# Optimization experiments

Measured on AMD Instinct MI355X. Metric: run time of the kernel, lower is better.

## Reference

```python
import jax, jax.numpy as jnp
import numpy as np

D_MODEL = 256
N_HEADS = 8
D_FF = 1024
N_LAYERS = 6
INPUT_DIM = 2
EPS = 1e-5  # torch LayerNorm default


def _layer_norm(x, g, b):
    m = jnp.mean(x, axis=-1, keepdims=True)
    v = jnp.mean((x - m) ** 2, axis=-1, keepdims=True)
    return (x - m) / jnp.sqrt(v + EPS) * g + b


def setup_inputs() -> dict:
    key = jax.random.key(0)
    ks = jax.random.split(key, 8)
    f32 = jnp.float32

    def w(k, shape, fan_in):
        return jax.random.normal(k, shape, f32) * (1.0 / np.sqrt(fan_in))

    return {
        "x": jax.random.normal(ks[0], (8, 1024, INPUT_DIM), f32),
        "in_w": w(ks[1], (INPUT_DIM, D_MODEL), INPUT_DIM),
        "in_b": jnp.zeros((D_MODEL,), f32),
        "ln1_g": jnp.ones((D_MODEL,), f32),
        "ln1_b": jnp.zeros((D_MODEL,), f32),
        "qkv_w": w(ks[2], (D_MODEL, 3 * D_MODEL), D_MODEL),
        "qkv_b": jnp.zeros((3 * D_MODEL,), f32),
        "out_w": w(ks[3], (D_MODEL, D_MODEL), D_MODEL),
        "out_b": jnp.zeros((D_MODEL,), f32),
        "lna_g": jnp.ones((D_MODEL,), f32),
        "lna_b": jnp.zeros((D_MODEL,), f32),
        "ln2_g": jnp.ones((D_MODEL,), f32),
        "ln2_b": jnp.zeros((D_MODEL,), f32),
        "ff1_w": w(ks[4], (D_MODEL, D_FF), D_MODEL),
        "ff1_b": jnp.zeros((D_FF,), f32),
        "ff2_w": w(ks[5], (D_FF, D_MODEL), D_FF),
        "ff2_b": jnp.zeros((D_MODEL,), f32),
        "lnf_g": jnp.ones((D_MODEL,), f32),
        "lnf_b": jnp.zeros((D_MODEL,), f32),
    }


def reference(x, in_w, in_b, ln1_g, ln1_b, qkv_w, qkv_b, out_w, out_b,
              lna_g, lna_b, ln2_g, ln2_b, ff1_w, ff1_b, ff2_w, ff2_b,
              lnf_g, lnf_b):
    B, L, _ = x.shape
    dk = D_MODEL // N_HEADS
    scale = 1.0 / np.sqrt(dk)
    top_k = max(1, L // 4)

    # sinusoidal positional encoding [L, D]
    pos = jnp.arange(L, dtype=jnp.float32)[:, None]
    div = jnp.exp(jnp.arange(0, D_MODEL, 2, dtype=jnp.float32)
                  * (-np.log(10000.0) / D_MODEL))
    pe = jnp.zeros((L, D_MODEL), jnp.float32)
    pe = pe.at[:, 0::2].set(jnp.sin(pos * div))
    pe = pe.at[:, 1::2].set(jnp.cos(pos * div))

    h = x @ in_w + in_b + pe[None]  # [B, L, D]

    # VoformerEncoder reuses the SAME layer object -> shared weights, 6 passes
    for _ in range(N_LAYERS):
        # --- self-attention sublayer (pre-norm) ---
        s2 = _layer_norm(h, ln1_g, ln1_b)
        qkv = (s2 @ qkv_w + qkv_b).reshape(B, L, 3, N_HEADS, dk)
        q = qkv[:, :, 0].transpose(0, 2, 1, 3)  # [B, H, L, dk]
        k = qkv[:, :, 1].transpose(0, 2, 1, 3)
        v = qkv[:, :, 2].transpose(0, 2, 1, 3)

        scores = jnp.einsum('bhqd,bhkd->bhqk', q, k) * scale  # [B,H,L,L]
        # ProbSparse: keep only the per-row top-k scores
        thr = jax.lax.top_k(scores, top_k)[0][..., -1:]
        sparse = jnp.where(scores >= thr, scores, -jnp.inf)
        attn = jax.nn.softmax(sparse, axis=-1)
        o = jnp.einsum('bhqk,bhkd->bhqd', attn, v)
        o = o.transpose(0, 2, 1, 3).reshape(B, L, D_MODEL)
        o = o @ out_w + out_b
        # InformerAttention applies its own residual + LayerNorm
        attn_out = _layer_norm(o + s2, lna_g, lna_b)
        h = h + attn_out

        # --- FFN sublayer with Volatilite activation ---
        s2 = _layer_norm(h, ln2_g, ln2_b)
        f = s2 @ ff1_w + ff1_b  # [B, L, d_ff]
        mean_f = jnp.mean(f, axis=1, keepdims=True)
        vol = jnp.sqrt(jnp.mean((mean_f - f) ** 2, axis=1, keepdims=True))
        f = f * vol
        f = f @ ff2_w + ff2_b
        h = h + f

    return _layer_norm(h, lnf_g, lnf_b)
```

## Files before the change

kernel.cpp:

```cpp
#include <hip/hip_runtime.h>
#include <hip/hip_bf16.h>
#include <math.h>

#define D_MODEL 256
#define NH 8
#define DFF 1024
#define NLAYERS 6
#define B_ 8
#define L_ 1024
#define NR (B_*L_)
#define TOPK 256
#define LNEPS 1e-5f

typedef __attribute__((ext_vector_type(8))) short bf16x8;
typedef __attribute__((ext_vector_type(4))) float f32x4;

__device__ __forceinline__ float wsum(float v){
  #pragma unroll
  for(int o=32;o>0;o>>=1) v += __shfl_xor(v,o,64);
  return v;
}
__device__ __forceinline__ short f2bf(float x){
  unsigned u = __float_as_uint(x);
  u += 0x7fffu + ((u>>16)&1u);
  return (short)(u>>16);
}
__device__ __forceinline__ float bf2f(short s){
  return __uint_as_float(((unsigned)(unsigned short)s)<<16);
}
__device__ __forceinline__ unsigned pk2bf(float a, float b){
  __hip_bfloat162 h = __float22bfloat162_rn(make_float2(a,b));
  unsigned u; __builtin_memcpy(&u, &h, 4);
  return u;
}
__device__ __forceinline__ float kinvf(int k){
  unsigned u = (k & 0x8000) ? ((unsigned)k ^ 0x8000u) : ((unsigned)k ^ 0xFFFFu);
  return __uint_as_float(u << 16);
}
__device__ __forceinline__ void g2l(const short* g, short* l){
  __builtin_amdgcn_global_load_lds(
      (const __attribute__((address_space(1))) unsigned int*)g,
      (__attribute__((address_space(3))) unsigned int*)l,
      16, 0, 0);
}

__global__ __launch_bounds__(256) void embed_kernel(
    const float* __restrict__ x, const float* __restrict__ in_w,
    const float* __restrict__ in_b, float* __restrict__ h)
{
  int tid = blockIdx.x*256 + threadIdx.x;
  int n  = tid >> 6;
  int d0 = (tid & 63) << 2;
  int l  = n & (L_-1);
  float x0 = x[2*n], x1 = x[2*n+1];
  const float kf = -0.07195578415606394f;
  float pe[4];
  #pragma unroll
  for(int ii=0; ii<2; ++ii){
    int i = (d0>>1) + ii;
    float dv  = expf((float)i * kf);
    float ang = (float)l * dv;
    pe[2*ii]   = sinf(ang);
    pe[2*ii+1] = cosf(ang);
  }
  float4 w0 = *(const float4*)(in_w + d0);
  float4 w1 = *(const float4*)(in_w + D_MODEL + d0);
  float4 bb = *(const float4*)(in_b + d0);
  float4 o;
  o.x = x0*w0.x + x1*w1.x + bb.x + pe[0];
  o.y = x0*w0.y + x1*w1.y + bb.y + pe[1];
  o.z = x0*w0.z + x1*w1.z + bb.z + pe[2];
  o.w = x0*w0.w + x1*w1.w + bb.w + pe[3];
  *(float4*)(h + (size_t)n*D_MODEL + d0) = o;
}

__global__ __launch_bounds__(256) void wcvt(
    const float* __restrict__ W, short* __restrict__ WT, int N, int kshift)
{
  int idx = blockIdx.x*256 + threadIdx.x;
  int K = 1<<kshift;
  if (idx >= N*K) return;
  int n = idx >> kshift, k = idx & (K-1);
  WT[idx] = f2bf(W[(size_t)k*N + n]);
}

template<int OM>
__global__ __launch_bounds__(256) void ln_kernel(
    const float* __restrict__ in, const float* __restrict__ g,
    const float* __restrict__ b, float* __restrict__ out,
    short* __restrict__ outb)
{
  int wave = threadIdx.x >> 6, lane = threadIdx.x & 63;
  int row = blockIdx.x*4 + wave;
  float4 v = ((const float4*)(in + (size_t)row*D_MODEL))[lane];
  float s  = v.x+v.y+v.z+v.w;
  float sq = v.x*v.x+v.y*v.y+v.z*v.z+v.w*v.w;
  s = wsum(s); sq = wsum(sq);
  float mean = s*(1.f/D_MODEL);
  float var  = sq*(1.f/D_MODEL) - mean*mean;
  float rstd = 1.f/sqrtf(var + LNEPS);
  float4 gv = ((const float4*)g)[lane];
  float4 bv = ((const float4*)b)[lane];
  float4 o;
  o.x = (v.x-mean)*rstd*gv.x + bv.x;
  o.y = (v.y-mean)*rstd*gv.y + bv.y;
  o.z = (v.z-mean)*rstd*gv.z + bv.z;
  o.w = (v.w-mean)*rstd*gv.w + bv.w;
  if (OM == 0){
    ((float4*)(out + (size_t)row*D_MODEL))[lane] = o;
  }
  if (OM == 2){
    uint2 pk; pk.x = pk2bf(o.x, o.y); pk.y = pk2bf(o.z, o.w);
    *(uint2*)(outb + (size_t)row*D_MODEL + lane*4) = pk;
  }
}

__global__ __launch_bounds__(256) void lnln_kernel(
    const float* __restrict__ tb,
    const float* __restrict__ ga, const float* __restrict__ ba,
    const float* __restrict__ g2, const float* __restrict__ b2,
    float* __restrict__ h, short* __restrict__ s2b)
{
  int wave = threadIdx.x >> 6, lane = threadIdx.x & 63;
  int row = blockIdx.x*4 + wave;
  float4 v = ((const float4*)(tb + (size_t)row*D_MODEL))[lane];
  float s  = v.x+v.y+v.z+v.w;
  float sq = v.x*v.x+v.y*v.y+v.z*v.z+v.w*v.w;
  s = wsum(s); sq = wsum(sq);
  float mean = s*(1.f/D_MODEL);
  float var  = sq*(1.f/D_MODEL) - mean*mean;
  float rstd = 1.f/sqrtf(var + LNEPS);
  float4 gv = ((const float4*)ga)[lane];
  float4 bv = ((const float4*)ba)[lane];
  float4* hp = (float4*)(h + (size_t)row*D_MODEL) + lane;
  float4 hv = *hp;
  float4 hn;
  hn.x = hv.x + (v.x-mean)*rstd*gv.x + bv.x;
  hn.y = hv.y + (v.y-mean)*rstd*gv.y + bv.y;
  hn.z = hv.z + (v.z-mean)*rstd*gv.z + bv.z;
  hn.w = hv.w + (v.w-mean)*rstd*gv.w + bv.w;
  *hp = hn;
  float s2  = hn.x+hn.y+hn.z+hn.w;
  float sq2 = hn.x*hn.x+hn.y*hn.y+hn.z*hn.z+hn.w*hn.w;
  s2 = wsum(s2); sq2 = wsum(sq2);
  float m2 = s2*(1.f/D_MODEL);
  float v2 = sq2*(1.f/D_MODEL) - m2*m2;
  float r2 = 1.f/sqrtf(v2 + LNEPS);
  float4 g2v = ((const float4*)g2)[lane];
  float4 b2v = ((const float4*)b2)[lane];
  uint2 pk;
  pk.x = pk2bf((hn.x-m2)*r2*g2v.x + b2v.x, (hn.y-m2)*r2*g2v.y + b2v.y);
  pk.y = pk2bf((hn.z-m2)*r2*g2v.z + b2v.z, (hn.w-m2)*r2*g2v.w + b2v.w);
  *(uint2*)(s2b + (size_t)row*D_MODEL + lane*4) = pk;
}

template<int MODE>
__global__ __launch_bounds__(256) void mfma_gemm(
    const short* __restrict__ A, const short* __restrict__ BT,
    const float* __restrict__ bias, const short* __restrict__ residb,
    float* __restrict__ Cf, short* __restrict__ Cb, short* __restrict__ Vt,
    int N, int K)
{
  __shared__ __align__(16) short As[128*32];
  __shared__ __align__(16) short Bs[64*32];
  const int t = threadIdx.x, wv = t>>6, lane = t&63;
  const int r16 = lane&15, quad = lane>>4;
  const int m0 = blockIdx.y*128, n0 = blockIdx.x*64;
  const int ia0 = wv*128 + lane, ia1 = ia0 + 64;
  const int ib  = wv*64 + lane;
  const short* Ab = A  + (size_t)m0*K;
  const short* Bb = BT + (size_t)n0*K;
  const f32x4 z = {0.f,0.f,0.f,0.f};
  f32x4 acc[2][4];
  #pragma unroll
  for (int i=0;i<2;++i)
    #pragma unroll
    for (int j=0;j<4;++j) acc[i][j] = z;

  for (int k0 = 0; k0 < K; k0 += 32){
    __syncthreads();
    g2l(Ab + (size_t)(ia0>>2)*K + k0 + (ia0&3)*8, As + ia0*8);
    g2l(Ab + (size_t)(ia1>>2)*K + k0 + (ia1&3)*8, As + ia1*8);
    g2l(Bb + (size_t)(ib>>2)*K  + k0 + (ib&3)*8,  Bs + ib*8);
    __syncthreads();
    bf16x8 af0 = *(const bf16x8*)(As + ((wv*32      + r16)*32 + quad*8));
    bf16x8 af1 = *(const bf16x8*)(As + ((wv*32 + 16 + r16)*32 + quad*8));
    bf16x8 bf[4];
    #pragma unroll
    for (int ct=0; ct<4; ++ct)
      bf[ct] = *(const bf16x8*)(Bs + ((ct*16 + r16)*32 + quad*8));
    #pragma unroll
    for (int ct=0; ct<4; ++ct){
      acc[0][ct] = __builtin_amdgcn_mfma_f32_16x16x32_bf16(af0, bf[ct], acc[0][ct], 0,0,0);
      acc[1][ct] = __builtin_amdgcn_mfma_f32_16x16x32_bf16(af1, bf[ct], acc[1][ct], 0,0,0);
    }
  }

  #pragma unroll
  for (int rt=0; rt<2; ++rt){
    const int mb = m0 + wv*32 + rt*16 + quad*4;
    #pragma unroll
    for (int ct=0; ct<4; ++ct){
      const int n = n0 + ct*16 + r16;
      const float bv = bias[n];
      if (MODE == 0){
        if (n < 512){
          int region = n>>8, hh = (n>>5)&7, d = n&31;
          #pragma unroll
          for (int r=0;r<4;++r){
            int l = mb + r;
            size_t base = (((size_t)(region*64 + (l>>10)*8 + hh))*1024 + (l&1023))*32 + d;
            Cb[base] = f2bf(acc[rt][ct][r] + bv);
          }
        } else {
          int dv = n - 512, hh = dv>>5, d = dv&31;
          int b = mb>>10, lloc = mb&1023;
          size_t base = (((size_t)(b*8 + hh))*32 + d)*1024 + lloc;
          uint2 pk;
          pk.x = pk2bf(acc[rt][ct][0] + bv, acc[rt][ct][1] + bv);
          pk.y = pk2bf(acc[rt][ct][2] + bv, acc[rt][ct][3] + bv);
          *(uint2*)(Vt + base) = pk;
        }
      } else {
        #pragma unroll
        for (int r=0;r<4;++r){
          size_t off = (size_t)(mb + r)*N + n;
          float c = acc[rt][ct][r] + bv;
          if (MODE == 1) Cf[off] = c + bf2f(residb[off]);
          if (MODE == 2) Cb[off] = f2bf(c);
          if (MODE == 3) Cf[off] += c;
        }
      }
    }
  }
}

__global__ __launch_bounds__(256,5) void attn_mfma(
    const short* __restrict__ qkbf, const short* __restrict__ vT,
    short* __restrict__ ob)
{
  __shared__ __align__(16) short sc16[16*1024];
  const int t = threadIdx.x, wv = t>>6, lane = t&63;
  const int r16 = lane&15, quad = lane>>4;
  const int blk = blockIdx.x;
  const int bh = (blk & 7)*8 + ((blk>>3)&7);
  const int qt = blk >> 6;

  bf16x8 aq = *(const bf16x8*)(qkbf + ((size_t)bh*1024 + qt*16 + r16)*32 + quad*8);
  const short* kb = qkbf + (size_t)(64 + bh)*1024*32;
  short* p0 = sc16 + quad*4096;

  #pragma unroll
  for (int g=0; g<4; ++g){
    bf16x8 bkb[4];
    #pragma unroll
    for (int j=0;j<4;++j)
      bkb[j] = *(const bf16x8*)(kb + (size_t)(wv*256 + (g*4+j)*16 + r16)*32 + quad*8);
    #pragma unroll
    for (int j=0;j<4;++j){
      f32x4 c = {0.f,0.f,0.f,0.f};
      c = __builtin_amdgcn_mfma_f32_16x16x32_bf16(aq, bkb[j], c, 0, 0, 0);
      const int keyq = (wv*256 + (g*4+j)*16 + r16) ^ ((quad&1)<<5);
      unsigned u01 = pk2bf(c[0], c[1]);
      unsigned u23 = pk2bf(c[2], c[3]);
      p0[keyq]               = (short)u01;
      p0[1024 + (keyq ^ 8)]  = (short)(u01>>16);
      p0[2048 + (keyq ^ 16)] = (short)u23;
      p0[3072 + (keyq ^ 24)] = (short)(u23>>16);
    }
  }
  __syncthreads();

  const float SC2 = 0.25500529485087056f;
  float iv0, iv1, iv2, iv3;
  #pragma unroll
  for (int rp=0; rp<2; ++rp){
    const int ra = wv*4 + rp*2;
    const int sa = (ra&7)<<3;
    short* pa = sc16 + ra*1024 + ((2*lane) ^ sa);
    short* pb = sc16 + (ra+1)*1024 + (((2*lane) ^ sa) ^ 8);
    float fa[16], fb[16];
    #pragma unroll
    for (int i=0;i<8;++i){
      unsigned wa = *(const unsigned*)(pa + i*128);
      unsigned wb = *(const unsigned*)(pb + i*128);
      fa[2*i]   = __uint_as_float(wa << 16);
      fa[2*i+1] = __uint_as_float(wa & 0xFFFF0000u);
      fb[2*i]   = __uint_as_float(wb << 16);
      fb[2*i+1] = __uint_as_float(wb & 0xFFFF0000u);
    }
    int loA = 0, loB = 0;
    #pragma unroll
    for (int bit = 15; bit >= 0; --bit){
      const int mA = loA | (1<<bit);
      const int mB = loB | (1<<bit);
      const float tA = kinvf(mA);
      const float tB = kinvf(mB);
      int cA = 0, cB = 0;
      #pragma unroll
      for (int i=0;i<16;++i){
        cA += (int)__popcll(__ballot(fa[i] >= tA));
        cB += (int)__popcll(__ballot(fb[i] >= tB));
      }
      if (cA >= TOPK) loA = mA;
      if (cB >= TOPK) loB = mB;
    }
    const float thrA = kinvf(loA), thrB = kinvf(loB);
    float suma = 0.f, sumb = 0.f;
    unsigned pka[8], pkb[8];
    #pragma unroll
    for (int i=0;i<8;++i){
      float ea0 = (fa[2*i]   >= thrA) ? exp2f(fa[2*i]  *SC2) : 0.f;
      float ea1 = (fa[2*i+1] >= thrA) ? exp2f(fa[2*i+1]*SC2) : 0.f;
      float eb0 = (fb[2*i]   >= thrB) ? exp2f(fb[2*i]  *SC2) : 0.f;
      float eb1 = (fb[2*i+1] >= thrB) ? exp2f(fb[2*i+1]*SC2) : 0.f;
      suma += ea0 + ea1; sumb += eb0 + eb1;
      pka[i] = pk2bf(ea0, ea1);
      pkb[i] = pk2bf(eb0, eb1);
    }
    suma = wsum(suma); sumb = wsum(sumb);
    if (rp == 0){ iv0 = 1.f/suma; iv1 = 1.f/sumb; }
    else        { iv2 = 1.f/suma; iv3 = 1.f/sumb; }
    #pragma unroll
    for (int i=0;i<8;++i){
      *(unsigned*)(pa + i*128) = pka[i];
      *(unsigned*)(pb + i*128) = pkb[i];
    }
  }
  const float invq = (quad==0)?iv0 : (quad==1)?iv1 : (quad==2)?iv2 : iv3;
  __syncthreads();

  const short* vb = vT + (size_t)bh*32*1024;
  const int sA = (r16&7) << 3;
  f32x4 oa0 = {0.f,0.f,0.f,0.f}, oa1 = {0.f,0.f,0.f,0.f};
  #pragma unroll
  for (int g=0; g<4; ++g){
    bf16x8 bvb[4];
    #pragma unroll
    for (int j=0;j<2;++j){
      int k0 = wv*256 + (g*2+j)*32;
      bvb[j*2+0] = *(const bf16x8*)(vb + (size_t)(     r16)*1024 + k0 + quad*8);
      bvb[j*2+1] = *(const bf16x8*)(vb + (size_t)(16 + r16)*1024 + k0 + quad*8);
    }
    #pragma unroll
    for (int j=0;j<2;++j){
      int k0 = wv*256 + (g*2+j)*32;
      bf16x8 af = *(const bf16x8*)(sc16 + r16*1024 + ((k0 + quad*8) ^ sA));
      oa0 = __builtin_amdgcn_mfma_f32_16x16x32_bf16(af, bvb[j*2+0], oa0, 0, 0, 0);
      oa1 = __builtin_amdgcn_mfma_f32_16x16x32_bf16(af, bvb[j*2+1], oa1, 0, 0, 0);
    }
  }
  __syncthreads();
  float* po = (float*)sc16;
  #pragma unroll
  for (int r=0;r<4;++r){
    po[wv*512 + (quad*4+r)*32 +      r16] = oa0[r];
    po[wv*512 + (quad*4+r)*32 + 16 + r16] = oa1[r];
  }
  __syncthreads();
  int e = t*2;
  float v0 = po[e]   + po[512+e]   + po[1024+e]   + po[1536+e];
  float v1 = po[e+1] + po[512+e+1] + po[1024+e+1] + po[1536+e+1];
  int q = e>>5, d = e&31;
  int b = bh>>3, hh = bh&7;
  size_t off = ((size_t)(b*1024 + qt*16 + q))*256 + hh*32 + d;
  *(unsigned*)(ob + off) = pk2bf(v0*invq, v1*invq);
}

__global__ __launch_bounds__(512) void vol_scale(short* __restrict__ f)
{
  __shared__ float ps[8][64], pq[8][64], vs[64];
  int b = blockIdx.x >> 4, cb = blockIdx.x & 15;
  int cl = threadIdx.x & 63, sl = threadIdx.x >> 6;
  int col = cb*64 + cl;
  short* fb = f + (size_t)b*L_*DFF + col;
  float s = 0.f, sq = 0.f;
  for (int l = sl*128; l < sl*128+128; ++l){
    float v = bf2f(fb[(size_t)l*DFF]);
    s += v; sq += v*v;
  }
  ps[sl][cl] = s; pq[sl][cl] = sq;
  __syncthreads();
  if (threadIdx.x < 64){
    float st=0.f, qt=0.f;
    #pragma unroll
    for (int i=0;i<8;++i){ st += ps[i][cl]; qt += pq[i][cl]; }
    float mean = st*(1.f/L_);
    float var  = qt*(1.f/L_) - mean*mean;
    vs[cl] = sqrtf(fmaxf(var, 0.f));
  }
  __syncthreads();
  float vv = vs[cl];
  for (int l = sl*128; l < sl*128+128; ++l){
    size_t o = (size_t)l*DFF;
    fb[o] = f2bf(bf2f(fb[o]) * vv);
  }
}

extern "C" void kernel_launch(void* const* d_in, const int* in_sizes, int n_in,
                              void* d_out, int out_size, void* d_ws, size_t ws_size,
                              hipStream_t stream) {
  const float* x     = (const float*)d_in[0];
  const float* in_w  = (const float*)d_in[1];
  const float* in_b  = (const float*)d_in[2];
  const float* ln1_g = (const float*)d_in[3];
  const float* ln1_b = (const float*)d_in[4];
  const float* qkv_w = (const float*)d_in[5];
  const float* qkv_b = (const float*)d_in[6];
  const float* out_w = (const float*)d_in[7];
  const float* out_b = (const float*)d_in[8];
  const float* lna_g = (const float*)d_in[9];
  const float* lna_b = (const float*)d_in[10];
  const float* ln2_g = (const float*)d_in[11];
  const float* ln2_b = (const float*)d_in[12];
  const float* ff1_w = (const float*)d_in[13];
  const float* ff1_b = (const float*)d_in[14];
  const float* ff2_w = (const float*)d_in[15];
  const float* ff2_b = (const float*)d_in[16];
  const float* lnf_g = (const float*)d_in[17];
  const float* lnf_b = (const float*)d_in[18];
  float* out = (float*)d_out;

  char* ws = (char*)d_ws;
  float* h     = (float*)(ws);
  short* s2b   = (short*)(ws + (size_t)( 8<<20));
  short* qkbf  = (short*)(ws + (size_t)(12<<20));
  short* vTb   = (short*)(ws + (size_t)(20<<20));
  short* ob_b  = (short*)(ws + (size_t)(24<<20));
  short* f     = (short*)(ws + (size_t)(12<<20));
  float* tb    = (float*)(ws + (size_t)(28<<20));
  short* qkvwT = (short*)(ws + (size_t)(36<<20));
  short* outwT = (short*)(ws + (size_t)(36<<20) + 393216);
  short* ff1wT = (short*)(ws + (size_t)(36<<20) + 393216 + 131072);
  short* ff2wT = (short*)(ws + (size_t)(36<<20) + 393216 + 131072 + 524288);

  embed_kernel<<<NR*64/256, 256, 0, stream>>>(x, in_w, in_b, h);
  wcvt<<< 768, 256, 0, stream>>>(qkv_w, qkvwT,  768, 8);
  wcvt<<< 256, 256, 0, stream>>>(out_w, outwT,  256, 8);
  wcvt<<<1024, 256, 0, stream>>>(ff1_w, ff1wT, 1024, 8);
  wcvt<<<1024, 256, 0, stream>>>(ff2_w, ff2wT,  256, 10);

  for (int layer = 0; layer < NLAYERS; ++layer){
    ln_kernel<2><<<NR/4, 256, 0, stream>>>(h, ln1_g, ln1_b, nullptr, s2b);
    {
      dim3 g(768/64, NR/128);
      mfma_gemm<0><<<g, 256, 0, stream>>>(s2b, qkvwT, qkv_b, nullptr,
                                          nullptr, qkbf, vTb, 768, 256);
    }
    attn_mfma<<<64*64, 256, 0, stream>>>(qkbf, vTb, ob_b);
    {
      dim3 g(256/64, NR/128);
      mfma_gemm<1><<<g, 256, 0, stream>>>(ob_b, outwT, out_b, s2b,
                                          tb, nullptr, nullptr, 256, 256);
    }
    lnln_kernel<<<NR/4, 256, 0, stream>>>(tb, lna_g, lna_b, ln2_g, ln2_b, h, s2b);
    {
      dim3 g(1024/64, NR/128);
      mfma_gemm<2><<<g, 256, 0, stream>>>(s2b, ff1wT, ff1_b, nullptr,
                                          nullptr, f, nullptr, 1024, 256);
    }
    vol_scale<<<B_*16, 512, 0, stream>>>(f);
    {
      dim3 g(256/64, NR/128);
      mfma_gemm<3><<<g, 256, 0, stream>>>(f, ff2wT, ff2_b, nullptr,
                                          h, nullptr, nullptr, 256, 1024);
    }
  }
  ln_kernel<0><<<NR/4, 256, 0, stream>>>(h, lnf_g, lnf_b, out, nullptr);
}
```

Before: 1.273 ms.

## Use 8 waves per attention block, one row pair per wave

The attention kernel now launches 512 threads (8 waves) per 16-query tile instead of 256. Each wave handles 128 keys in the score and PV stages and one pair of rows in the top-k/softmax stage, where before it handled two pairs. Normalization is now applied to the probabilities before the PV MFMA rather than to the output. A separate 16KB LDS buffer for the partial-output reduction removes one barrier, at the cost of more shared memory per block and an 8-way reduction done by half the threads.

```diff
diff --git a/kernel.cpp b/kernel.cpp
--- a/kernel.cpp
+++ b/kernel.cpp
@@ -235,11 +235,12 @@
   }
 }
 
-__global__ __launch_bounds__(256,5) void attn_mfma(
+__global__ __launch_bounds__(512,6) void attn_mfma(
     const short* __restrict__ qkbf, const short* __restrict__ vT,
     short* __restrict__ ob)
 {
   __shared__ __align__(16) short sc16[16*1024];
+  __shared__ __align__(16) float po[8*512];
   const int t = threadIdx.x, wv = t>>6, lane = t&63;
   const int r16 = lane&15, quad = lane>>4;
   const int blk = blockIdx.x;
@@ -251,16 +252,16 @@
   short* p0 = sc16 + quad*4096;
 
   #pragma unroll
-  for (int g=0; g<4; ++g){
+  for (int g=0; g<2; ++g){
     bf16x8 bkb[4];
     #pragma unroll
     for (int j=0;j<4;++j)
-      bkb[j] = *(const bf16x8*)(kb + (size_t)(wv*256 + (g*4+j)*16 + r16)*32 + quad*8);
+      bkb[j] = *(const bf16x8*)(kb + (size_t)(wv*128 + (g*4+j)*16 + r16)*32 + quad*8);
     #pragma unroll
     for (int j=0;j<4;++j){
       f32x4 c = {0.f,0.f,0.f,0.f};
       c = __builtin_amdgcn_mfma_f32_16x16x32_bf16(aq, bkb[j], c, 0, 0, 0);
-      const int keyq = (wv*256 + (g*4+j)*16 + r16) ^ ((quad&1)<<5);
+      const int keyq = (wv*128 + (g*4+j)*16 + r16) ^ ((quad&1)<<5);
       unsigned u01 = pk2bf(c[0], c[1]);
       unsigned u23 = pk2bf(c[2], c[3]);
       p0[keyq]               = (short)u01;
@@ -272,10 +273,8 @@
   __syncthreads();
 
   const float SC2 = 0.25500529485087056f;
-  float iv0, iv1, iv2, iv3;
-  #pragma unroll
-  for (int rp=0; rp<2; ++rp){
-    const int ra = wv*4 + rp*2;
+  {
+    const int ra = wv*2;
     const int sa = (ra&7)<<3;
     short* pa = sc16 + ra*1024 + ((2*lane) ^ sa);
     short* pb = sc16 + (ra+1)*1024 + (((2*lane) ^ sa) ^ 8);
@@ -306,65 +305,52 @@
       if (cB >= TOPK) loB = mB;
     }
     const float thrA = kinvf(loA), thrB = kinvf(loB);
+    float ea[16], eb[16];
     float suma = 0.f, sumb = 0.f;
-    unsigned pka[8], pkb[8];
+    #pragma unroll
+    for (int i=0;i<16;++i){
+      ea[i] = (fa[i] >= thrA) ? exp2f(fa[i]*SC2) : 0.f;
+      eb[i] = (fb[i] >= thrB) ? exp2f(fb[i]*SC2) : 0.f;
+      suma += ea[i]; sumb += eb[i];
+    }
+    suma = wsum(suma); sumb = wsum(sumb);
+    const float inva = 1.f/suma, invb = 1.f/sumb;
     #pragma unroll
     for (int i=0;i<8;++i){
-      float ea0 = (fa[2*i]   >= thrA) ? exp2f(fa[2*i]  *SC2) : 0.f;
-      float ea1 = (fa[2*i+1] >= thrA) ? exp2f(fa[2*i+1]*SC2) : 0.f;
-      float eb0 = (fb[2*i]   >= thrB) ? exp2f(fb[2*i]  *SC2) : 0.f;
-      float eb1 = (fb[2*i+1] >= thrB) ? exp2f(fb[2*i+1]*SC2) : 0.f;
-      suma += ea0 + ea1; sumb += eb0 + eb1;
-      pka[i] = pk2bf(ea0, ea1);
-      pkb[i] = pk2bf(eb0, eb1);
-    }
-    suma = wsum(suma); sumb = wsum(sumb);
-    if (rp == 0){ iv0 = 1.f/suma; iv1 = 1.f/sumb; }
-    else        { iv2 = 1.f/suma; iv3 = 1.f/sumb; }
-    #pragma unroll
-    for (int i=0;i<8;++i){
-      *(unsigned*)(pa + i*128) = pka[i];
-      *(unsigned*)(pb + i*128) = pkb[i];
-    }
-  }
-  const float invq = (quad==0)?iv0 : (quad==1)?iv1 : (quad==2)?iv2 : iv3;
+      *(unsigned*)(pa + i*128) = pk2bf(ea[2*i]*inva, ea[2*i+1]*inva);
+      *(unsigned*)(pb + i*128) = pk2bf(eb[2*i]*invb, eb[2*i+1]*invb);
+    }
+  }
   __syncthreads();
 
   const short* vb = vT + (size_t)bh*32*1024;
   const int sA = (r16&7) << 3;
   f32x4 oa0 = {0.f,0.f,0.f,0.f}, oa1 = {0.f,0.f,0.f,0.f};
   #pragma unroll
-  for (int g=0; g<4; ++g){
-    bf16x8 bvb[4];
-    #pragma unroll
-    for (int j=0;j<2;++j){
-      int k0 = wv*256 + (g*2+j)*32;
-      bvb[j*2+0] = *(const bf16x8*)(vb + (size_t)(     r16)*1024 + k0 + quad*8);
-      bvb[j*2+1] = *(const bf16x8*)(vb + (size_t)(16 + r16)*1024 + k0 + quad*8);
-    }
-    #pragma unroll
-    for (int j=0;j<2;++j){
-      int k0 = wv*256 + (g*2+j)*32;
-      bf16x8 af = *(const bf16x8*)(sc16 + r16*1024 + ((k0 + quad*8) ^ sA));
-      oa0 = __builtin_amdgcn_mfma_f32_16x16x32_bf16(af, bvb[j*2+0], oa0, 0, 0, 0);
-      oa1 = __builtin_amdgcn_mfma_f32_16x16x32_bf16(af, bvb[j*2+1], oa1, 0, 0, 0);
-    }
-  }
-  __syncthreads();
-  float* po = (float*)sc16;
+  for (int j=0;j<4;++j){
+    int k0 = wv*128 + j*32;
+    bf16x8 b0 = *(const bf16x8*)(vb + (size_t)(     r16)*1024 + k0 + quad*8);
+    bf16x8 b1 = *(const bf16x8*)(vb + (size_t)(16 + r16)*1024 + k0 + quad*8);
+    bf16x8 af = *(const bf16x8*)(sc16 + r16*1024 + ((k0 + quad*8) ^ sA));
+    oa0 = __builtin_amdgcn_mfma_f32_16x16x32_bf16(af, b0, oa0, 0, 0, 0);
+    oa1 = __builtin_amdgcn_mfma_f32_16x16x32_bf16(af, b1, oa1, 0, 0, 0);
+  }
   #pragma unroll
   for (int r=0;r<4;++r){
     po[wv*512 + (quad*4+r)*32 +      r16] = oa0[r];
     po[wv*512 + (quad*4+r)*32 + 16 + r16] = oa1[r];
   }
   __syncthreads();
-  int e = t*2;
-  float v0 = po[e]   + po[512+e]   + po[1024+e]   + po[1536+e];
-  float v1 = po[e+1] + po[512+e+1] + po[1024+e+1] + po[1536+e+1];
-  int q = e>>5, d = e&31;
-  int b = bh>>3, hh = bh&7;
-  size_t off = ((size_t)(b*1024 + qt*16 + q))*256 + hh*32 + d;
-  *(unsigned*)(ob + off) = pk2bf(v0*invq, v1*invq);
+  if (t < 256){
+    int e = t*2;
+    float v0 = 0.f, v1 = 0.f;
+    #pragma unroll
+    for (int w=0;w<8;++w){ v0 += po[w*512 + e]; v1 += po[w*512 + e + 1]; }
+    int q = e>>5, d = e&31;
+    int b = bh>>3, hh = bh&7;
+    size_t off = ((size_t)(b*1024 + qt*16 + q))*256 + hh*32 + d;
+    *(unsigned*)(ob + off) = pk2bf(v0, v1);
+  }
 }
 
 __global__ __launch_bounds__(512) void vol_scale(short* __restrict__ f)
@@ -447,7 +433,7 @@
       mfma_gemm<0><<<g, 256, 0, stream>>>(s2b, qkvwT, qkv_b, nullptr,
                                           nullptr, qkbf, vTb, 768, 256);
     }
-    attn_mfma<<<64*64, 256, 0, stream>>>(qkbf, vTb, ob_b);
+    attn_mfma<<<64*64, 512, 0, stream>>>(qkbf, vTb, ob_b);
     {
       dim3 g(256/64, NR/128);
       mfma_gemm<1><<<g, 256, 0, stream>>>(ob_b, outwT, out_b, s2b,
```

Result: faster. 1.180 ms (-7.2%).
